# Kernel optimization log

Measured on AMD Instinct MI355X. Metric: run time of the kernel, lower is better.

The kernel has to match this reference:

```python
import jax, jax.numpy as jnp
import numpy as np

_NUM_RBF = 8
_R_MAX = 3.0  # randn point clouds have radius ~ sqrt(3)
_CENTERS = jnp.linspace(0.0, _R_MAX, _NUM_RBF)
_C15 = float(np.sqrt(15.0))
_C5 = float(np.sqrt(5.0))


def _sph_basis(positions):
    """map_3d_feats_to_basis_functions: 8x0e (radial RBFs) + 1x1o (l=1 SH) + 1x2e (l=2 SH)."""
    centered = positions - jnp.mean(positions, axis=-2, keepdims=True)  # [B,N,3]
    r = jnp.sqrt(jnp.sum(centered * centered, axis=-1) + 1e-12)         # [B,N]
    d = centered / r[..., None]                                         # unit directions
    x, y, z = d[..., 0], d[..., 1], d[..., 2]
    s0 = jnp.exp(-(r[..., None] - _CENTERS) ** 2)                       # [B,N,8] scalar feats (0e)
    sh1 = d                                                             # [B,N,3] (1o)
    sh2 = jnp.stack([_C15 * x * y,
                     _C15 * y * z,
                     0.5 * _C5 * (3.0 * z * z - 1.0),
                     _C15 * x * z,
                     0.5 * _C15 * (x * x - y * y)], axis=-1)            # [B,N,5] (2e)
    return s0, sh1, sh2


def _mix(feat, W):
    # Equivariant per-l channel mixing: feat [B, mul_in, dim_l], W [mul_in, mul_out]
    return jnp.einsum('bci,co->boi', feat, W) / jnp.sqrt(jnp.asarray(W.shape[0], feat.dtype))


def reference(positions, W1a, W1b, W1c, W1d, W2a, W2b, W2c):
    s0, sh1, sh2 = _sph_basis(positions)
    # avg_irreps_with_same_id: average over the N points axis
    s = jnp.mean(s0, axis=-2)[..., None]          # [B,8,1]  8x0e
    v = jnp.mean(sh1, axis=-2)[:, None, :]        # [B,1,3]  1x1o
    # (mean of sh2 is dropped: linear1 output has no 2e)
    # linear1: '8x0e+1x1o+1x2e' -> '6x0e+4x1o' -> '6x0e+4x1o'
    s = _mix(_mix(s, W1a), W1b)                   # [B,6,1]
    v = _mix(_mix(v, W1c), W1d)                   # [B,4,3]
    # linear2: '6x0e+4x1o' -> '6x0e+4x1o' -> '6x0e'
    s = _mix(_mix(s, W2a), W2b)                   # [B,6,1]
    _ = _mix(v, W2c)                              # mid 1o channel, dropped by '6x0e' output
    # torch.cat of the six 0e irreps -> [B,6]
    return s[..., 0]


def setup_inputs() -> dict:
    key = jax.random.key(0)
    ks = jax.random.split(key, 8)
    return {
        'positions': jax.random.normal(ks[0], (32768, 128, 3), dtype=jnp.float32),
        'W1a': jax.random.normal(ks[1], (8, 6), dtype=jnp.float32),
        'W1b': jax.random.normal(ks[2], (6, 6), dtype=jnp.float32),
        'W1c': jax.random.normal(ks[3], (1, 4), dtype=jnp.float32),
        'W1d': jax.random.normal(ks[4], (4, 4), dtype=jnp.float32),
        'W2a': jax.random.normal(ks[5], (6, 6), dtype=jnp.float32),
        'W2b': jax.random.normal(ks[6], (6, 6), dtype=jnp.float32),
        'W2c': jax.random.normal(ks[7], (4, 4), dtype=jnp.float32),
    }
```

## Files before the change

kernel.cpp:

```cpp
#include <hip/hip_runtime.h>


template <int N>
__device__ __forceinline__ float ror16(float v) {
    return __int_as_float(__builtin_amdgcn_update_dpp(
        0, __float_as_int(v), 0x120 | N, 0xF, 0xF, true));
}
__device__ __forceinline__ float rowsum16(float v) {
    v += ror16<1>(v);
    v += ror16<2>(v);
    v += ror16<4>(v);
    v += ror16<8>(v);
    return v;
}

__global__ __launch_bounds__(256, 4) void sph_fused(
    const float* __restrict__ pos,
    const float* __restrict__ W1a, const float* __restrict__ W1b,
    const float* __restrict__ W2a, const float* __restrict__ W2b,
    float* __restrict__ out, int nBatch)
{
    __shared__ float BBs[36];
    __shared__ float CCs[36];
    __shared__ float MMs[48];

    const int t = threadIdx.x;

    if (t < 36) {
        const int c = t / 6, o = t - 6 * c;
        float s = 0.f;
        #pragma unroll
        for (int j = 0; j < 6; ++j) s += W2a[c * 6 + j] * W2b[j * 6 + o];
        BBs[t] = s;
    }
    __syncthreads();
    if (t < 36) {
        const int c = t / 6, o = t - 6 * c;
        float s = 0.f;
        #pragma unroll
        for (int j = 0; j < 6; ++j) s += W1b[c * 6 + j] * BBs[j * 6 + o];
        CCs[t] = s;
    }
    __syncthreads();
    if (t < 48) {
        const int k = t / 6, o = t - 6 * k;
        float s = 0.f;
        #pragma unroll
        for (int c = 0; c < 6; ++c) s += W1a[k * 6 + c] * CCs[c * 6 + o];
        MMs[t] = s * (0.024056261216234408f / 128.0f);
    }
    __syncthreads();

    const int lane = t & 63;
    const int w    = t >> 6;
    const int lsub = lane & 15;
    const int grp  = lane >> 4;

    const int col = (lsub < 6) ? lsub : 0;
    float Mcol[8];
    #pragma unroll
    for (int k = 0; k < 8; ++k) Mcol[k] = MMs[k * 6 + col];

    const int nTiles = (nBatch + 3) >> 2;
    const int nWaves = gridDim.x * 4;
    int tile = blockIdx.x * 4 + w;
    if (tile >= nTiles) return;

    const float4* __restrict__ p4 = reinterpret_cast<const float4*>(pos);
    const int maxC = nBatch * 96 - 6;

    union Pts { float4 q[6]; float f[24]; };
    Pts A, B;

    const float WK1 = 0.83220583f, WK2 = 0.47965235f, WK3 = 0.19146295f,
                WK4 = 0.05293049f, WK5 = 0.01013418f, WK6 = 0.00134381f,
                WK7 = 1.2340980e-4f;

#define LOADT(U, T) do {                                                   \
    int base_ = (T) * 384 + grp * 96 + lsub * 6;                           \
    if (base_ > maxC) base_ = maxC;    \
    _Pragma("unroll")                                                      \
    for (int j_ = 0; j_ < 6; ++j_) (U).q[j_] = p4[base_ + j_];             \
} while (0)

#define COMPUTE(U, T) do {                                                 \
    float sx_ = 0.f, sy_ = 0.f, sz_ = 0.f;                                 \
    _Pragma("unroll")                                                      \
    for (int i_ = 0; i_ < 8; ++i_) {                                       \
        sx_ += (U).f[3 * i_ + 0];                                          \
        sy_ += (U).f[3 * i_ + 1];                                          \
        sz_ += (U).f[3 * i_ + 2];                                          \
    }                                                                      \
    sx_ = rowsum16(sx_); sy_ = rowsum16(sy_); sz_ = rowsum16(sz_);         \
    const float mx_ = sx_ * (1.f / 128.f);                                 \
    const float my_ = sy_ * (1.f / 128.f);                                 \
    const float mz_ = sz_ * (1.f / 128.f);                                 \
    float a0_=0.f,a1_=0.f,a2_=0.f,a3_=0.f,a4_=0.f,a5_=0.f,a6_=0.f,a7_=0.f; \
    _Pragma("unroll")                                                      \
    for (int i_ = 0; i_ < 8; ++i_) {                                       \
        const float dx_ = (U).f[3 * i_ + 0] - mx_;                         \
        const float dy_ = (U).f[3 * i_ + 1] - my_;                         \
        const float dz_ = (U).f[3 * i_ + 2] - mz_;                         \
        const float r2_ = fmaf(dx_, dx_, fmaf(dy_, dy_, fmaf(dz_, dz_, 1e-12f))); \
        float r_;                                                          \
        asm("v_sqrt_f32 %0, %1" : "=v"(r_) : "v"(r2_));                    \
        const float E0_ = __expf(-r2_);                                    \
        const float Bf_ = __expf(r_ * (6.0f / 7.0f));                      \
        float p_ = E0_;                                                    \
        a0_ += E0_;                                                        \
        p_ *= Bf_; a1_ = fmaf(p_, WK1, a1_);                               \
        p_ *= Bf_; a2_ = fmaf(p_, WK2, a2_);                               \
        p_ *= Bf_; a3_ = fmaf(p_, WK3, a3_);                               \
        p_ *= Bf_; a4_ = fmaf(p_, WK4, a4_);                               \
        p_ *= Bf_; a5_ = fmaf(p_, WK5, a5_);                               \
        p_ *= Bf_; a6_ = fmaf(p_, WK6, a6_);                               \
        p_ *= Bf_; a7_ = fmaf(p_, WK7, a7_);                               \
    }                                                                      \
    a0_ = rowsum16(a0_); a1_ = rowsum16(a1_);                              \
    a2_ = rowsum16(a2_); a3_ = rowsum16(a3_);                              \
    a4_ = rowsum16(a4_); a5_ = rowsum16(a5_);                              \
    a6_ = rowsum16(a6_); a7_ = rowsum16(a7_);                              \
    float o_ = a0_ * Mcol[0];                                              \
    o_ = fmaf(a1_, Mcol[1], o_); o_ = fmaf(a2_, Mcol[2], o_);              \
    o_ = fmaf(a3_, Mcol[3], o_); o_ = fmaf(a4_, Mcol[4], o_);              \
    o_ = fmaf(a5_, Mcol[5], o_); o_ = fmaf(a6_, Mcol[6], o_);              \
    o_ = fmaf(a7_, Mcol[7], o_);                                           \
    const int batch_ = (T) * 4 + grp;                                      \
    if (lsub < 6 && batch_ < nBatch) out[batch_ * 6 + lsub] = o_;          \
} while (0)

    LOADT(A, tile);
    for (;;) {
        int tn = tile + nWaves;
        if (tn < nTiles) {
            LOADT(B, tn);
            COMPUTE(A, tile);
        } else {
            COMPUTE(A, tile);
            break;
        }
        tile = tn; tn = tile + nWaves;
        if (tn < nTiles) {
            LOADT(A, tn);
            COMPUTE(B, tile);
        } else {
            COMPUTE(B, tile);
            break;
        }
        tile = tn;
    }
#undef LOADT
#undef COMPUTE
}

extern "C" void kernel_launch(void* const* d_in, const int* in_sizes, int n_in,
                              void* d_out, int out_size, void* d_ws, size_t ws_size,
                              hipStream_t stream) {
    const float* pos = (const float*)d_in[0];
    const float* W1a = (const float*)d_in[1];
    const float* W1b = (const float*)d_in[2];
    const float* W2a = (const float*)d_in[5];
    const float* W2b = (const float*)d_in[6];
    float* out = (float*)d_out;

    const int nBatch = in_sizes[0] / 384;
    const int nTiles = (nBatch + 3) / 4;
    int grid = (nTiles + 3) / 4;
    if (grid > 1024) grid = 1024;

    sph_fused<<<dim3(grid), dim3(256), 0, stream>>>(pos, W1a, W1b, W2a, W2b, out, nBatch);
}
```

Measured before the change: 15.55 us.

## Replace persistent double-buffered loop with one tile per wave and fold RBF weights

Drops the persistent grid-stride loop with its manual double-buffered loads and launches one wave per 4-batch tile, so the grid scales with the batch count instead of being capped at 1024 blocks. The per-k RBF polynomial weights are folded into the shared mixing matrix, which turns the per-point fmas into plain adds, and the occupancy hint is raised to 8 blocks per CU. This trades explicit load/compute overlap for more resident waves to hide memory latency, but adds per-block setup cost since every block recomputes the small weight products.

```diff
diff --git a/kernel.cpp b/kernel.cpp
--- a/kernel.cpp
+++ b/kernel.cpp
@@ -14,7 +14,7 @@
     return v;
 }
 
-__global__ __launch_bounds__(256, 4) void sph_fused(
+__global__ __launch_bounds__(256, 8) void sph_fused(
     const float* __restrict__ pos,
     const float* __restrict__ W1a, const float* __restrict__ W1b,
     const float* __restrict__ W2a, const float* __restrict__ W2b,
@@ -47,7 +47,9 @@
         float s = 0.f;
         #pragma unroll
         for (int c = 0; c < 6; ++c) s += W1a[k * 6 + c] * CCs[c * 6 + o];
-        MMs[t] = s * (0.024056261216234408f / 128.0f);
+        const float WKtab[8] = {1.0f, 0.83220583f, 0.47965235f, 0.19146295f,
+                                0.05293049f, 0.01013418f, 0.00134381f, 1.2340980e-4f};
+        MMs[t] = s * WKtab[k] * (0.024056261216234408f / 128.0f);
     }
     __syncthreads();
 
@@ -56,101 +58,64 @@
     const int lsub = lane & 15;
     const int grp  = lane >> 4;
 
-    const int col = (lsub < 6) ? lsub : 0;
-    float Mcol[8];
-    #pragma unroll
-    for (int k = 0; k < 8; ++k) Mcol[k] = MMs[k * 6 + col];
-
     const int nTiles = (nBatch + 3) >> 2;
-    const int nWaves = gridDim.x * 4;
-    int tile = blockIdx.x * 4 + w;
+    const int tile = blockIdx.x * 4 + w;
     if (tile >= nTiles) return;
 
     const float4* __restrict__ p4 = reinterpret_cast<const float4*>(pos);
+    int base = tile * 384 + grp * 96 + lsub * 6;
     const int maxC = nBatch * 96 - 6;
+    if (base > maxC) base = maxC;
 
-    union Pts { float4 q[6]; float f[24]; };
-    Pts A, B;
+    union { float4 q[6]; float f[24]; } u;
+    #pragma unroll
+    for (int j = 0; j < 6; ++j) u.q[j] = p4[base + j];
 
-    const float WK1 = 0.83220583f, WK2 = 0.47965235f, WK3 = 0.19146295f,
-                WK4 = 0.05293049f, WK5 = 0.01013418f, WK6 = 0.00134381f,
-                WK7 = 1.2340980e-4f;
+    float sx = 0.f, sy = 0.f, sz = 0.f;
+    #pragma unroll
+    for (int i = 0; i < 8; ++i) {
+        sx += u.f[3 * i + 0]; sy += u.f[3 * i + 1]; sz += u.f[3 * i + 2];
+    }
+    sx = rowsum16(sx); sy = rowsum16(sy); sz = rowsum16(sz);
+    const float mx = sx * (1.f / 128.f), my = sy * (1.f / 128.f), mz = sz * (1.f / 128.f);
 
-#define LOADT(U, T) do {                                                   \
-    int base_ = (T) * 384 + grp * 96 + lsub * 6;                           \
-    if (base_ > maxC) base_ = maxC;    \
-    _Pragma("unroll")                                                      \
-    for (int j_ = 0; j_ < 6; ++j_) (U).q[j_] = p4[base_ + j_];             \
-} while (0)
+    float a0 = 0.f, a1 = 0.f, a2 = 0.f, a3 = 0.f,
+          a4 = 0.f, a5 = 0.f, a6 = 0.f, a7 = 0.f;
+    #pragma unroll
+    for (int i = 0; i < 8; ++i) {
+        const float dx = u.f[3 * i + 0] - mx;
+        const float dy = u.f[3 * i + 1] - my;
+        const float dz = u.f[3 * i + 2] - mz;
+        const float r2 = fmaf(dx, dx, fmaf(dy, dy, fmaf(dz, dz, 1e-12f)));
+        float r;
+        asm("v_sqrt_f32 %0, %1" : "=v"(r) : "v"(r2));
+        const float E0 = __expf(-r2);
+        const float Bf = __expf(r * (6.0f / 7.0f));
+        float p = E0;
+        a0 += E0;
+        p *= Bf; a1 += p;
+        p *= Bf; a2 += p;
+        p *= Bf; a3 += p;
+        p *= Bf; a4 += p;
+        p *= Bf; a5 += p;
+        p *= Bf; a6 += p;
+        p *= Bf; a7 += p;
+    }
+    a0 = rowsum16(a0); a1 = rowsum16(a1); a2 = rowsum16(a2); a3 = rowsum16(a3);
+    a4 = rowsum16(a4); a5 = rowsum16(a5); a6 = rowsum16(a6); a7 = rowsum16(a7);
 
-#define COMPUTE(U, T) do {                                                 \
-    float sx_ = 0.f, sy_ = 0.f, sz_ = 0.f;                                 \
-    _Pragma("unroll")                                                      \
-    for (int i_ = 0; i_ < 8; ++i_) {                                       \
-        sx_ += (U).f[3 * i_ + 0];                                          \
-        sy_ += (U).f[3 * i_ + 1];                                          \
-        sz_ += (U).f[3 * i_ + 2];                                          \
-    }                                                                      \
-    sx_ = rowsum16(sx_); sy_ = rowsum16(sy_); sz_ = rowsum16(sz_);         \
-    const float mx_ = sx_ * (1.f / 128.f);                                 \
-    const float my_ = sy_ * (1.f / 128.f);                                 \
-    const float mz_ = sz_ * (1.f / 128.f);                                 \
-    float a0_=0.f,a1_=0.f,a2_=0.f,a3_=0.f,a4_=0.f,a5_=0.f,a6_=0.f,a7_=0.f; \
-    _Pragma("unroll")                                                      \
-    for (int i_ = 0; i_ < 8; ++i_) {                                       \
-        const float dx_ = (U).f[3 * i_ + 0] - mx_;                         \
-        const float dy_ = (U).f[3 * i_ + 1] - my_;                         \
-        const float dz_ = (U).f[3 * i_ + 2] - mz_;                         \
-        const float r2_ = fmaf(dx_, dx_, fmaf(dy_, dy_, fmaf(dz_, dz_, 1e-12f))); \
-        float r_;                                                          \
-        asm("v_sqrt_f32 %0, %1" : "=v"(r_) : "v"(r2_));                    \
-        const float E0_ = __expf(-r2_);                                    \
-        const float Bf_ = __expf(r_ * (6.0f / 7.0f));                      \
-        float p_ = E0_;                                                    \
-        a0_ += E0_;                                                        \
-        p_ *= Bf_; a1_ = fmaf(p_, WK1, a1_);                               \
-        p_ *= Bf_; a2_ = fmaf(p_, WK2, a2_);                               \
-        p_ *= Bf_; a3_ = fmaf(p_, WK3, a3_);                               \
-        p_ *= Bf_; a4_ = fmaf(p_, WK4, a4_);                               \
-        p_ *= Bf_; a5_ = fmaf(p_, WK5, a5_);                               \
-        p_ *= Bf_; a6_ = fmaf(p_, WK6, a6_);                               \
-        p_ *= Bf_; a7_ = fmaf(p_, WK7, a7_);                               \
-    }                                                                      \
-    a0_ = rowsum16(a0_); a1_ = rowsum16(a1_);                              \
-    a2_ = rowsum16(a2_); a3_ = rowsum16(a3_);                              \
-    a4_ = rowsum16(a4_); a5_ = rowsum16(a5_);                              \
-    a6_ = rowsum16(a6_); a7_ = rowsum16(a7_);                              \
-    float o_ = a0_ * Mcol[0];                                              \
-    o_ = fmaf(a1_, Mcol[1], o_); o_ = fmaf(a2_, Mcol[2], o_);              \
-    o_ = fmaf(a3_, Mcol[3], o_); o_ = fmaf(a4_, Mcol[4], o_);              \
-    o_ = fmaf(a5_, Mcol[5], o_); o_ = fmaf(a6_, Mcol[6], o_);              \
-    o_ = fmaf(a7_, Mcol[7], o_);                                           \
-    const int batch_ = (T) * 4 + grp;                                      \
-    if (lsub < 6 && batch_ < nBatch) out[batch_ * 6 + lsub] = o_;          \
-} while (0)
+    const int col = (lsub < 6) ? lsub : 0;
+    float o_ = a0 * MMs[0 * 6 + col];
+    o_ = fmaf(a1, MMs[1 * 6 + col], o_);
+    o_ = fmaf(a2, MMs[2 * 6 + col], o_);
+    o_ = fmaf(a3, MMs[3 * 6 + col], o_);
+    o_ = fmaf(a4, MMs[4 * 6 + col], o_);
+    o_ = fmaf(a5, MMs[5 * 6 + col], o_);
+    o_ = fmaf(a6, MMs[6 * 6 + col], o_);
+    o_ = fmaf(a7, MMs[7 * 6 + col], o_);
 
-    LOADT(A, tile);
-    for (;;) {
-        int tn = tile + nWaves;
-        if (tn < nTiles) {
-            LOADT(B, tn);
-            COMPUTE(A, tile);
-        } else {
-            COMPUTE(A, tile);
-            break;
-        }
-        tile = tn; tn = tile + nWaves;
-        if (tn < nTiles) {
-            LOADT(A, tn);
-            COMPUTE(B, tile);
-        } else {
-            COMPUTE(B, tile);
-            break;
-        }
-        tile = tn;
-    }
-#undef LOADT
-#undef COMPUTE
+    const int batch = tile * 4 + grp;
+    if (lsub < 6 && batch < nBatch) out[batch * 6 + lsub] = o_;
 }
 
 extern "C" void kernel_launch(void* const* d_in, const int* in_sizes, int n_in,
@@ -165,8 +130,7 @@
 
     const int nBatch = in_sizes[0] / 384;
     const int nTiles = (nBatch + 3) / 4;
-    int grid = (nTiles + 3) / 4;
-    if (grid > 1024) grid = 1024;
+    const int grid = (nTiles + 3) / 4;
 
     sph_fused<<<dim3(grid), dim3(256), 0, stream>>>(pos, W1a, W1b, W2a, W2b, out, nBatch);
 }
```

Measured after the change: 14.96 us. 1.04x faster.
